# Kernel tuning notes

Measured on AMD Instinct MI355X. Metric: run time of the kernel, lower is better.

The kernel has to match this reference:

```python
import jax, jax.numpy as jnp
import numpy as np

N = 50000
E = 800000
D_IN = 256
D1, D2, D3 = 256, 256, 128


def setup_inputs() -> dict:
    key = jax.random.key(0)
    ks = jax.random.split(key, 9)
    qe = jax.random.normal(ks[0], (N, D_IN), dtype=jnp.float32)
    obj = jax.random.normal(ks[1], (N, D_IN), dtype=jnp.float32)
    edge_index = jax.random.randint(ks[2], (2, E), 0, N, dtype=jnp.int64)
    def glorot(k, fan_in, fan_out):
        s = jnp.sqrt(6.0 / (fan_in + fan_out)).astype(jnp.float32)
        return jax.random.uniform(k, (fan_in, fan_out), jnp.float32, -s, s)
    return {
        "question_embedding": qe,
        "object_features": obj,
        "edge_index": edge_index,
        "W1": glorot(ks[3], D_IN, D1), "b1": jnp.zeros((D1,), jnp.float32),
        "W2": glorot(ks[4], D1, D2),  "b2": jnp.zeros((D2,), jnp.float32),
        "W3": glorot(ks[5], D2, D3),  "b3": jnp.zeros((D3,), jnp.float32),
    }


def _gcn_norm(edge_index, num_nodes):
    # PyG GCNConv default: add self-loops, symmetric normalization D^-1/2 (A+I) D^-1/2
    loop = jnp.arange(num_nodes, dtype=edge_index.dtype)
    row = jnp.concatenate([edge_index[0], loop])  # destination
    col = jnp.concatenate([edge_index[1], loop])  # source
    ones = jnp.ones(row.shape[0], dtype=jnp.float32)
    deg = jax.ops.segment_sum(ones, row, num_segments=num_nodes)
    dinv = jnp.where(deg > 0, jax.lax.rsqrt(deg), 0.0)
    norm = dinv[row] * dinv[col]  # [E+N]
    return row, col, norm


def _gcn_layer(x, W, b, row, col, norm, num_nodes):
    h = x @ W                                   # [N, d_out] dense transform first (smaller msgs)
    msgs = norm[:, None] * h[col]               # gather + scale: [E+N, d_out]
    out = jax.ops.segment_sum(msgs, row, num_segments=num_nodes)  # scatter-add
    return out + b


def reference(question_embedding, object_features, edge_index, W1, b1, W2, b2, W3, b3):
    # Hadamard fusion of question embedding with per-object features (MuRel-style)
    x = question_embedding * object_features
    row, col, norm = _gcn_norm(edge_index, N)
    x = jax.nn.relu(_gcn_layer(x, W1, b1, row, col, norm, N))
    x = jax.nn.relu(_gcn_layer(x, W2, b2, row, col, norm, N))
    x = _gcn_layer(x, W3, b3, row, col, norm, N)
    return x
```

## Files before the change

### kernel.cpp

```cpp
#include <hip/hip_runtime.h>
#include <cstdint>
#include <cstddef>

#define NN 50000
#define NE 800000
#define NBLK ((NN + 255) / 256)

typedef _Float16 f16x8 __attribute__((ext_vector_type(8)));
typedef _Float16 f16x4 __attribute__((ext_vector_type(4)));
typedef float f32x4 __attribute__((ext_vector_type(4)));

__device__ __forceinline__ int edge_at(const void* e, int is32, long long i) {
    return is32 ? ((const int*)e)[i] : (int)((const long long*)e)[i];
}

__global__ __launch_bounds__(64) void zero_flag_k(int* flag) {
    if (threadIdx.x == 0) *flag = 0;
}

__global__ __launch_bounds__(256) void detect_k(const int* __restrict__ w, int* __restrict__ flag) {
    int i = blockIdx.x * 256 + threadIdx.x;
    if (i < 1024 && w[2 * i + 1] != 0) atomicOr(flag, 1);
}

__global__ __launch_bounds__(256) void init_k(int* __restrict__ deg, int* __restrict__ cursor, int n) {
    int i = blockIdx.x * 256 + threadIdx.x;
    if (i < n) { deg[i] = 1; cursor[i] = 0; }
}

__global__ __launch_bounds__(256) void count_k(const void* __restrict__ edges,
                                               const int* __restrict__ flag,
                                               int* __restrict__ deg, int e) {
    int i = blockIdx.x * 256 + threadIdx.x;
    if (i < e) {
        int is32 = *flag;
        atomicAdd(&deg[edge_at(edges, is32, i)], 1);
    }
}

__global__ __launch_bounds__(256) void bh_k(const int* __restrict__ deg,
                                            int* __restrict__ bh, int n) {
    __shared__ int lh[1024];
    int t = threadIdx.x;
    for (int b = t; b < 1024; b += 256) lh[b] = 0;
    __syncthreads();
    int i = blockIdx.x * 256 + t;
    if (i < n) atomicAdd(&lh[min(deg[i], 1023)], 1);
    __syncthreads();
    for (int b = t; b < 1024; b += 256) bh[(size_t)blockIdx.x * 1024 + b] = lh[b];
}

__global__ __launch_bounds__(256) void btot_k(const int* __restrict__ bh,
                                              int* __restrict__ tot, int nb) {
    __shared__ int red[256];
    int b = blockIdx.x, t = threadIdx.x;
    int s = 0;
    for (int blk = t; blk < nb; blk += 256) s += bh[(size_t)blk * 1024 + b];
    red[t] = s;
    __syncthreads();
    for (int off = 128; off; off >>= 1) {
        if (t < off) red[t] += red[t + off];
        __syncthreads();
    }
    if (t == 0) tot[b] = red[0];
}

__global__ __launch_bounds__(1024) void hscan_k(const int* __restrict__ hist,
                                                int* __restrict__ bcur) {
    __shared__ int s[1024];
    int t = threadIdx.x;
    s[t] = hist[t];
    __syncthreads();
    for (int off = 1; off < 1024; off <<= 1) {
        int val = (t >= off) ? s[t - off] : 0;
        __syncthreads();
        s[t] += val;
        __syncthreads();
    }
    bcur[t] = (t == 0) ? 0 : s[t - 1];
}

__global__ __launch_bounds__(256) void bbase_k(int* __restrict__ bh,
                                               const int* __restrict__ bstart, int nb) {
    __shared__ int s[256];
    int b = blockIdx.x, t = threadIdx.x;
    int v = (t < nb) ? bh[(size_t)t * 1024 + b] : 0;
    s[t] = v;
    __syncthreads();
    for (int off = 1; off < 256; off <<= 1) {
        int x = (t >= off) ? s[t - off] : 0;
        __syncthreads();
        s[t] += x;
        __syncthreads();
    }
    int excl = (t == 0) ? 0 : s[t - 1];
    if (t < nb) bh[(size_t)t * 1024 + b] = bstart[b] + excl;
}

__global__ __launch_bounds__(256) void pscatter_k(const int* __restrict__ deg,
                                                  const int* __restrict__ bh,
                                                  int* __restrict__ perm,
                                                  int* __restrict__ inv_perm, int n) {
    __shared__ int lh[1024];
    int t = threadIdx.x;
    for (int b = t; b < 1024; b += 256) lh[b] = 0;
    __syncthreads();
    int i = blockIdx.x * 256 + t;
    int b = 0, r = 0;
    if (i < n) {
        b = min(deg[i], 1023);
        r = atomicAdd(&lh[b], 1);
    }
    __syncthreads();
    if (i < n) {
        int pos = bh[(size_t)blockIdx.x * 1024 + b] + r;
        perm[pos] = i;
        inv_perm[i] = pos;
    }
}

__global__ __launch_bounds__(256) void degs_k(const int* __restrict__ deg,
                                              const int* __restrict__ perm,
                                              int* __restrict__ deg_s,
                                              float* __restrict__ dinv_s, int n) {
    int i = blockIdx.x * 256 + threadIdx.x;
    if (i < n) {
        int d = deg[perm[i]];
        deg_s[i] = d;
        dinv_s[i] = rsqrtf((float)d);
    }
}

__global__ __launch_bounds__(256) void ppart_k(const int* __restrict__ deg,
                                               int* __restrict__ part, int n) {
    __shared__ int red[256];
    int t = threadIdx.x;
    int i = blockIdx.x * 256 + t;
    red[t] = (i < n) ? deg[i] - 1 : 0;
    __syncthreads();
    for (int off = 128; off; off >>= 1) {
        if (t < off) red[t] += red[t + off];
        __syncthreads();
    }
    if (t == 0) part[blockIdx.x] = red[0];
}

__global__ __launch_bounds__(256) void pscan1_k(int* __restrict__ part, int nb) {
    __shared__ int s[256];
    int t = threadIdx.x;
    s[t] = (t < nb) ? part[t] : 0;
    __syncthreads();
    for (int off = 1; off < 256; off <<= 1) {
        int v = (t >= off) ? s[t - off] : 0;
        __syncthreads();
        s[t] += v;
        __syncthreads();
    }
    if (t < nb) part[t] = (t == 0) ? 0 : s[t - 1];
}

__global__ __launch_bounds__(256) void pwrite_k(const int* __restrict__ deg,
                                                const int* __restrict__ part,
                                                int* __restrict__ rp, int n) {
    __shared__ int s[256];
    int t = threadIdx.x;
    int i = blockIdx.x * 256 + t;
    int val = (i < n) ? deg[i] - 1 : 0;
    s[t] = val;
    __syncthreads();
    for (int off = 1; off < 256; off <<= 1) {
        int v = (t >= off) ? s[t - off] : 0;
        __syncthreads();
        s[t] += v;
        __syncthreads();
    }
    int incl = s[t];
    if (i < n) rp[i] = part[blockIdx.x] + incl - val;
    if (i == n - 1) rp[n] = part[blockIdx.x] + incl;
}

__global__ __launch_bounds__(256) void scatter_k(const void* __restrict__ edges,
                                                 const int* __restrict__ flag,
                                                 const int* __restrict__ inv_perm,
                                                 const int* __restrict__ rp,
                                                 int* __restrict__ cursor,
                                                 unsigned short* __restrict__ col_s, int e) {
    int i = blockIdx.x * 256 + threadIdx.x;
    if (i < e) {
        int is32 = *flag;
        int r = inv_perm[edge_at(edges, is32, i)];
        int c = inv_perm[edge_at(edges, is32, (long long)NE + i)];
        int pos = rp[r] + atomicAdd(&cursor[r], 1);
        col_s[pos] = (unsigned short)c;
    }
}

__global__ __launch_bounds__(256) void hadamard_k(const float4* __restrict__ a,
                                                  const float4* __restrict__ b,
                                                  const int* __restrict__ perm,
                                                  _Float16* __restrict__ Xh,
                                                  _Float16* __restrict__ Xl, int n4) {
    int i = blockIdx.x * 256 + threadIdx.x;
    if (i >= n4) return;
    int slot = i >> 6;
    int q = i & 63;
    int v = perm[slot];
    float4 x = a[(size_t)v * 64 + q], y = b[(size_t)v * 64 + q];
    float vv[4] = { x.x * y.x, x.y * y.y, x.z * y.z, x.w * y.w };
    f16x4 hh, ll;
    #pragma unroll
    for (int j = 0; j < 4; ++j) {
        _Float16 h = (_Float16)vv[j];
        hh[j] = h;
        ll[j] = (_Float16)(vv[j] - (float)h);
    }
    int cq = q * 4;
    size_t off = ((size_t)(cq >> 5) * NN + slot) * 32 + (cq & 31);
    *(f16x4*)&Xh[off] = hh;
    *(f16x4*)&Xl[off] = ll;
}

__global__ __launch_bounds__(256) void wconv_k(const float* __restrict__ W,
                                               _Float16* __restrict__ B3,
                                               int Nout, int nseg) {
    int n = blockIdx.x;
    int k = threadIdx.x;
    float v = W[(size_t)k * Nout + n];
    _Float16 h = (_Float16)v;
    _Float16 l = (_Float16)(v - (float)h);
    size_t base = (size_t)n * (nseg * 256);
    B3[base + k]       = h;
    B3[base + 256 + k] = l;
    if (nseg == 3) B3[base + 512 + k] = h;
}

__device__ __forceinline__ void gload_lds16(const void* g, void* l) {
    __builtin_amdgcn_global_load_lds(
        (const __attribute__((address_space(1))) void*)g,
        (__attribute__((address_space(3))) void*)l, 16, 0, 0);
}

template <int NBX, int SW, int NSEG>
__global__ __launch_bounds__(256) void gemm_f16_k(const _Float16* __restrict__ Ah,
                                                  const _Float16* __restrict__ Al,
                                                  const _Float16* __restrict__ B3,
                                                  const float* __restrict__ dinv_s,
                                                  _Float16* __restrict__ C,
                                                  int M, int Nout) {
    __shared__ alignas(16) _Float16 sA[128 * 32];
    __shared__ alignas(16) _Float16 sB[128 * 32];
    constexpr int LG = (SW == 32) ? 5 : 4;
    constexpr int NST = NSEG * 8;
    constexpr int BSTR = NSEG * 256;
    int mblk = (M + 127) >> 7;

    int pair, xb;
    if (NBX == 2) {
        int b = blockIdx.x;
        pair = (b >> 4) * 8 + (b & 7);
        xb   = (b >> 3) & 1;
        if (pair >= mblk) return;
    } else {
        pair = blockIdx.x;
        xb = 0;
    }

    int tid = threadIdx.x;
    int row0 = pair * 128, col0 = xb * 128;
    int wid = tid >> 6, lane = tid & 63;
    int wm = wid >> 1, wn = wid & 1;
    int fr = lane & 15;
    int kbc = lane >> 4;

    int sr = lane >> 2;
    int ke = (((lane & 3) ^ ((sr >> 1) & 3)) * 8);

    f32x4 acc[4][4] = {};

    for (int s = 0; s < NST; ++s) {
        int p = s & 7;
        const _Float16* Asrc = Ah;
        if constexpr (NSEG == 3) {
            if ((s >> 3) == 2) Asrc = Al;
        }

        __syncthreads();
        #pragma unroll
        for (int c = 0; c < 2; ++c) {
            int ch = wid * 2 + c;
            int r = ch * 16 + sr;
            int arow = row0 + r;
            if (arow < M)
                gload_lds16(&Asrc[((size_t)p * M + arow) * 32 + ke], &sA[ch * 512]);
            gload_lds16(&B3[(size_t)(col0 + r) * BSTR + s * 32 + ke], &sB[ch * 512]);
        }
        __syncthreads();

        f16x8 af[4];
        #pragma unroll
        for (int f = 0; f < 4; ++f) {
            int rr = wm * 64 + f * 16 + fr;
            af[f] = *(const f16x8*)&sA[rr * 32 + ((kbc ^ ((rr >> 1) & 3)) * 8)];
        }
        #pragma unroll
        for (int g = 0; g < 4; ++g) {
            int cc = wn * 64 + g * 16 + fr;
            f16x8 bf_ = *(const f16x8*)&sB[cc * 32 + ((kbc ^ ((cc >> 1) & 3)) * 8)];
            #pragma unroll
            for (int f = 0; f < 4; ++f)
                acc[f][g] = __builtin_amdgcn_mfma_f32_16x16x32_f16(af[f], bf_, acc[f][g], 0, 0, 0);
        }
    }

    int rsub = (lane >> 4) * 4;
    float dsc[4][4];
    #pragma unroll
    for (int f = 0; f < 4; ++f)
        #pragma unroll
        for (int r = 0; r < 4; ++r) {
            int row = row0 + wm * 64 + f * 16 + rsub + r;
            dsc[f][r] = (row < M) ? dinv_s[row] : 0.0f;
        }
    #pragma unroll
    for (int f = 0; f < 4; ++f) {
        #pragma unroll
        for (int g = 0; g < 4; ++g) {
            int col = col0 + wn * 64 + g * 16 + fr;
            #pragma unroll
            for (int r = 0; r < 4; ++r) {
                int row = row0 + wm * 64 + f * 16 + rsub + r;
                if (row < M)
                    C[((size_t)(col >> LG) * M + row) * SW + (col & (SW - 1))] =
                        (_Float16)(acc[f][g][r] * dsc[f][r]);
            }
        }
    }
}

template <int D, int MODE>
__global__ __launch_bounds__(256) void aggregate_slice_k(const _Float16* __restrict__ G,
                                                         const float* __restrict__ bias,
                                                         const float* __restrict__ dinv_s,
                                                         const int* __restrict__ rp,
                                                         const unsigned short* __restrict__ cs,
                                                         const int* __restrict__ perm,
                                                         _Float16* __restrict__ Yh,
                                                         float* __restrict__ Yf, int n) {
    constexpr int SLICE = (D == 256) ? 32 : 16;
    constexpr int LPN = SLICE / 8;
    constexpr int NPB = 256 / LPN;

    int bid = blockIdx.x;
    int s = bid & 7;
    int slot = (bid >> 3) * NPB + threadIdx.x / LPN;
    if (slot >= n) return;
    int sub = threadIdx.x % LPN;
    int co = sub * 8;
    int col = s * SLICE + co;

    const _Float16* Gs = G + (size_t)s * n * SLICE;

    float acc[8];
    {
        f16x8 t0 = *(const f16x8*)&Gs[(size_t)slot * SLICE + co];
        #pragma unroll
        for (int i = 0; i < 8; ++i) acc[i] = (float)t0[i];
    }

    int beg = rp[slot], end = rp[slot + 1];
    int j = beg;
    for (; j + 8 <= end; j += 8) {
        int cc[8];
        #pragma unroll
        for (int u = 0; u < 8; ++u) cc[u] = cs[j + u];
        f16x8 hv[8];
        #pragma unroll
        for (int u = 0; u < 8; ++u)
            hv[u] = *(const f16x8*)&Gs[(size_t)cc[u] * SLICE + co];
        #pragma unroll
        for (int u = 0; u < 8; ++u)
            #pragma unroll
            for (int i = 0; i < 8; ++i)
                acc[i] += (float)hv[u][i];
    }
    for (; j < end; ++j) {
        int c = cs[j];
        f16x8 a = *(const f16x8*)&Gs[(size_t)c * SLICE + co];
        #pragma unroll
        for (int i = 0; i < 8; ++i) acc[i] += (float)a[i];
    }

    float dv = dinv_s[slot];
    float4 b0 = *(const float4*)&bias[col];
    float4 b1 = *(const float4*)&bias[col + 4];
    float bb[8] = { b0.x, b0.y, b0.z, b0.w, b1.x, b1.y, b1.z, b1.w };

    if constexpr (MODE == 0) {
        f16x8 hh;
        #pragma unroll
        for (int i = 0; i < 8; ++i)
            hh[i] = (_Float16)fmaxf(dv * acc[i] + bb[i], 0.0f);
        size_t off = ((size_t)s * n + slot) * SLICE + co;
        *(f16x8*)&Yh[off] = hh;
    } else {
        int v = perm[slot];
        float o[8];
        #pragma unroll
        for (int i = 0; i < 8; ++i) o[i] = dv * acc[i] + bb[i];
        *(float4*)&Yf[(size_t)v * D + col]     = make_float4(o[0], o[1], o[2], o[3]);
        *(float4*)&Yf[(size_t)v * D + col + 4] = make_float4(o[4], o[5], o[6], o[7]);
    }
}

extern "C" void kernel_launch(void* const* d_in, const int* in_sizes, int n_in,
                              void* d_out, int out_size, void* d_ws, size_t ws_size,
                              hipStream_t stream) {
    const float* qe  = (const float*)d_in[0];
    const float* obj = (const float*)d_in[1];
    const void*  edges = d_in[2];
    const float* W1 = (const float*)d_in[3];
    const float* b1 = (const float*)d_in[4];
    const float* W2 = (const float*)d_in[5];
    const float* b2 = (const float*)d_in[6];
    const float* W3 = (const float*)d_in[7];
    const float* b3 = (const float*)d_in[8];
    float* out = (float*)d_out;

    char* p = (char*)d_ws;
    _Float16* Xh   = (_Float16*)p; p += (size_t)NN * 256 * 2;
    _Float16* Xl   = (_Float16*)p; p += (size_t)NN * 256 * 2;
    _Float16* H    = (_Float16*)p; p += (size_t)NN * 256 * 2;
    _Float16* B3   = (_Float16*)p; p += (size_t)256 * 768 * 2;
    int*   deg     = (int*)p;   p += (size_t)NN * 4;
    int*   deg_s   = (int*)p;   p += (size_t)NN * 4;
    float* dinv_s  = (float*)p; p += (size_t)NN * 4;
    int*   rp      = (int*)p;   p += (size_t)(NN + 1) * 4;
    int*   cursor  = (int*)p;   p += (size_t)NN * 4;
    unsigned short* col_s = (unsigned short*)p; p += (size_t)NE * 2;
    int*   bh      = (int*)p;   p += (size_t)NBLK * 1024 * 4;
    int*   tot     = (int*)p;   p += 1024 * 4;
    int*   bstart  = (int*)p;   p += 1024 * 4;
    int*   part    = (int*)p;   p += NBLK * 4;
    int*   perm    = (int*)p;   p += (size_t)NN * 4;
    int*   inv_perm= (int*)p;   p += (size_t)NN * 4;
    int*   flag    = (int*)p;   p += 4;

    zero_flag_k<<<1, 64, 0, stream>>>(flag);
    detect_k<<<4, 256, 0, stream>>>((const int*)edges, flag);
    init_k<<<(NN + 255) / 256, 256, 0, stream>>>(deg, cursor, NN);
    count_k<<<(NE + 255) / 256, 256, 0, stream>>>(edges, flag, deg, NE);
    bh_k<<<NBLK, 256, 0, stream>>>(deg, bh, NN);
    btot_k<<<1024, 256, 0, stream>>>(bh, tot, NBLK);
    hscan_k<<<1, 1024, 0, stream>>>(tot, bstart);
    bbase_k<<<1024, 256, 0, stream>>>(bh, bstart, NBLK);
    pscatter_k<<<NBLK, 256, 0, stream>>>(deg, bh, perm, inv_perm, NN);
    degs_k<<<NBLK, 256, 0, stream>>>(deg, perm, deg_s, dinv_s, NN);
    ppart_k<<<NBLK, 256, 0, stream>>>(deg_s, part, NN);
    pscan1_k<<<1, 256, 0, stream>>>(part, NBLK);
    pwrite_k<<<NBLK, 256, 0, stream>>>(deg_s, part, rp, NN);
    scatter_k<<<(NE + 255) / 256, 256, 0, stream>>>(edges, flag, inv_perm, rp, cursor,
                                                    col_s, NE);
    hadamard_k<<<(NN * 64 + 255) / 256, 256, 0, stream>>>(
        (const float4*)qe, (const float4*)obj, perm, Xh, Xl, NN * 64);

    int mblk = (NN + 127) / 128;
    int gemmBigGrid = ((mblk + 7) / 8) * 16;
    int agg256Grid = ((NN + 63) / 64) * 8;
    int agg128Grid = ((NN + 127) / 128) * 8;

    wconv_k<<<256, 256, 0, stream>>>(W1, B3, 256, 3);
    gemm_f16_k<2, 32, 3><<<gemmBigGrid, 256, 0, stream>>>(Xh, Xl, B3, dinv_s, H, NN, 256);
    aggregate_slice_k<256, 0><<<agg256Grid, 256, 0, stream>>>(H, b1, dinv_s, rp, col_s, perm,
                                                              Xh, nullptr, NN);
    wconv_k<<<256, 256, 0, stream>>>(W2, B3, 256, 2);
    gemm_f16_k<2, 32, 2><<<gemmBigGrid, 256, 0, stream>>>(Xh, nullptr, B3, dinv_s, H, NN, 256);
    aggregate_slice_k<256, 0><<<agg256Grid, 256, 0, stream>>>(H, b2, dinv_s, rp, col_s, perm,
                                                              Xh, nullptr, NN);
    wconv_k<<<128, 256, 0, stream>>>(W3, B3, 128, 2);
    gemm_f16_k<1, 16, 2><<<mblk, 256, 0, stream>>>(Xh, nullptr, B3, dinv_s, H, NN, 128);
    aggregate_slice_k<128, 1><<<agg128Grid, 256, 0, stream>>>(H, b3, dinv_s, rp, col_s, perm,
                                                              nullptr, out, NN);
}
```

Measured before the change: 356.5 us.

## Drop low-half activation split in layer 1 and double-buffer GEMM LDS stages

Result: faster. 342.7 us (-3.9%).

```diff
diff --git a/kernel.cpp b/kernel.cpp
--- a/kernel.cpp
+++ b/kernel.cpp
@@ -198,40 +198,31 @@
 __global__ __launch_bounds__(256) void hadamard_k(const float4* __restrict__ a,
                                                   const float4* __restrict__ b,
                                                   const int* __restrict__ perm,
-                                                  _Float16* __restrict__ Xh,
-                                                  _Float16* __restrict__ Xl, int n4) {
+                                                  _Float16* __restrict__ Xh, int n4) {
     int i = blockIdx.x * 256 + threadIdx.x;
     if (i >= n4) return;
     int slot = i >> 6;
     int q = i & 63;
     int v = perm[slot];
     float4 x = a[(size_t)v * 64 + q], y = b[(size_t)v * 64 + q];
-    float vv[4] = { x.x * y.x, x.y * y.y, x.z * y.z, x.w * y.w };
-    f16x4 hh, ll;
-    #pragma unroll
-    for (int j = 0; j < 4; ++j) {
-        _Float16 h = (_Float16)vv[j];
-        hh[j] = h;
-        ll[j] = (_Float16)(vv[j] - (float)h);
-    }
+    f16x4 hh;
+    hh[0] = (_Float16)(x.x * y.x);
+    hh[1] = (_Float16)(x.y * y.y);
+    hh[2] = (_Float16)(x.z * y.z);
+    hh[3] = (_Float16)(x.w * y.w);
     int cq = q * 4;
     size_t off = ((size_t)(cq >> 5) * NN + slot) * 32 + (cq & 31);
     *(f16x4*)&Xh[off] = hh;
-    *(f16x4*)&Xl[off] = ll;
 }
 
 __global__ __launch_bounds__(256) void wconv_k(const float* __restrict__ W,
-                                               _Float16* __restrict__ B3,
-                                               int Nout, int nseg) {
+                                               _Float16* __restrict__ B3, int Nout) {
     int n = blockIdx.x;
     int k = threadIdx.x;
     float v = W[(size_t)k * Nout + n];
     _Float16 h = (_Float16)v;
-    _Float16 l = (_Float16)(v - (float)h);
-    size_t base = (size_t)n * (nseg * 256);
-    B3[base + k]       = h;
-    B3[base + 256 + k] = l;
-    if (nseg == 3) B3[base + 512 + k] = h;
+    B3[(size_t)n * 512 + k]       = h;
+    B3[(size_t)n * 512 + 256 + k] = (_Float16)(v - (float)h);
 }
 
 __device__ __forceinline__ void gload_lds16(const void* g, void* l) {
@@ -240,18 +231,16 @@
         (__attribute__((address_space(3))) void*)l, 16, 0, 0);
 }
 
-template <int NBX, int SW, int NSEG>
+template <int NBX, int SW>
 __global__ __launch_bounds__(256) void gemm_f16_k(const _Float16* __restrict__ Ah,
-                                                  const _Float16* __restrict__ Al,
                                                   const _Float16* __restrict__ B3,
                                                   const float* __restrict__ dinv_s,
                                                   _Float16* __restrict__ C,
                                                   int M, int Nout) {
-    __shared__ alignas(16) _Float16 sA[128 * 32];
-    __shared__ alignas(16) _Float16 sB[128 * 32];
+    __shared__ alignas(16) _Float16 sA[2][128 * 32];
+    __shared__ alignas(16) _Float16 sB[2][128 * 32];
     constexpr int LG = (SW == 32) ? 5 : 4;
-    constexpr int NST = NSEG * 8;
-    constexpr int BSTR = NSEG * 256;
+    constexpr int NST = 16;
     int mblk = (M + 127) >> 7;
 
     int pair, xb;
@@ -277,39 +266,43 @@
 
     f32x4 acc[4][4] = {};
 
-    for (int s = 0; s < NST; ++s) {
+    auto STAGE = [&](int bsel, int s) {
         int p = s & 7;
-        const _Float16* Asrc = Ah;
-        if constexpr (NSEG == 3) {
-            if ((s >> 3) == 2) Asrc = Al;
-        }
-
-        __syncthreads();
         #pragma unroll
         for (int c = 0; c < 2; ++c) {
             int ch = wid * 2 + c;
             int r = ch * 16 + sr;
             int arow = row0 + r;
             if (arow < M)
-                gload_lds16(&Asrc[((size_t)p * M + arow) * 32 + ke], &sA[ch * 512]);
-            gload_lds16(&B3[(size_t)(col0 + r) * BSTR + s * 32 + ke], &sB[ch * 512]);
+                gload_lds16(&Ah[((size_t)p * M + arow) * 32 + ke], &sA[bsel][ch * 512]);
+            gload_lds16(&B3[(size_t)(col0 + r) * 512 + s * 32 + ke], &sB[bsel][ch * 512]);
         }
-        __syncthreads();
+    };
+
+    STAGE(0, 0);
+    __syncthreads();
+    int cur = 0;
+
+    for (int s = 0; s < NST; ++s) {
+        if (s + 1 < NST) STAGE(cur ^ 1, s + 1);
 
         f16x8 af[4];
         #pragma unroll
         for (int f = 0; f < 4; ++f) {
             int rr = wm * 64 + f * 16 + fr;
-            af[f] = *(const f16x8*)&sA[rr * 32 + ((kbc ^ ((rr >> 1) & 3)) * 8)];
+            af[f] = *(const f16x8*)&sA[cur][rr * 32 + ((kbc ^ ((rr >> 1) & 3)) * 8)];
         }
         #pragma unroll
         for (int g = 0; g < 4; ++g) {
             int cc = wn * 64 + g * 16 + fr;
-            f16x8 bf_ = *(const f16x8*)&sB[cc * 32 + ((kbc ^ ((cc >> 1) & 3)) * 8)];
+            f16x8 bf_ = *(const f16x8*)&sB[cur][cc * 32 + ((kbc ^ ((cc >> 1) & 3)) * 8)];
             #pragma unroll
             for (int f = 0; f < 4; ++f)
                 acc[f][g] = __builtin_amdgcn_mfma_f32_16x16x32_f16(af[f], bf_, acc[f][g], 0, 0, 0);
         }
+
+        __syncthreads();
+        cur ^= 1;
     }
 
     int rsub = (lane >> 4) * 4;
@@ -428,9 +421,8 @@
 
     char* p = (char*)d_ws;
     _Float16* Xh   = (_Float16*)p; p += (size_t)NN * 256 * 2;
-    _Float16* Xl   = (_Float16*)p; p += (size_t)NN * 256 * 2;
     _Float16* H    = (_Float16*)p; p += (size_t)NN * 256 * 2;
-    _Float16* B3   = (_Float16*)p; p += (size_t)256 * 768 * 2;
+    _Float16* B3   = (_Float16*)p; p += (size_t)256 * 512 * 2;
     int*   deg     = (int*)p;   p += (size_t)NN * 4;
     int*   deg_s   = (int*)p;   p += (size_t)NN * 4;
     float* dinv_s  = (float*)p; p += (size_t)NN * 4;
@@ -461,23 +453,23 @@
     scatter_k<<<(NE + 255) / 256, 256, 0, stream>>>(edges, flag, inv_perm, rp, cursor,
                                                     col_s, NE);
     hadamard_k<<<(NN * 64 + 255) / 256, 256, 0, stream>>>(
-        (const float4*)qe, (const float4*)obj, perm, Xh, Xl, NN * 64);
+        (const float4*)qe, (const float4*)obj, perm, Xh, NN * 64);
 
     int mblk = (NN + 127) / 128;
     int gemmBigGrid = ((mblk + 7) / 8) * 16;
     int agg256Grid = ((NN + 63) / 64) * 8;
     int agg128Grid = ((NN + 127) / 128) * 8;
 
-    wconv_k<<<256, 256, 0, stream>>>(W1, B3, 256, 3);
-    gemm_f16_k<2, 32, 3><<<gemmBigGrid, 256, 0, stream>>>(Xh, Xl, B3, dinv_s, H, NN, 256);
+    wconv_k<<<256, 256, 0, stream>>>(W1, B3, 256);
+    gemm_f16_k<2, 32><<<gemmBigGrid, 256, 0, stream>>>(Xh, B3, dinv_s, H, NN, 256);
     aggregate_slice_k<256, 0><<<agg256Grid, 256, 0, stream>>>(H, b1, dinv_s, rp, col_s, perm,
                                                               Xh, nullptr, NN);
-    wconv_k<<<256, 256, 0, stream>>>(W2, B3, 256, 2);
-    gemm_f16_k<2, 32, 2><<<gemmBigGrid, 256, 0, stream>>>(Xh, nullptr, B3, dinv_s, H, NN, 256);
+    wconv_k<<<256, 256, 0, stream>>>(W2, B3, 256);
+    gemm_f16_k<2, 32><<<gemmBigGrid, 256, 0, stream>>>(Xh, B3, dinv_s, H, NN, 256);
     aggregate_slice_k<256, 0><<<agg256Grid, 256, 0, stream>>>(H, b2, dinv_s, rp, col_s, perm,
                                                               Xh, nullptr, NN);
-    wconv_k<<<128, 256, 0, stream>>>(W3, B3, 128, 2);
-    gemm_f16_k<1, 16, 2><<<mblk, 256, 0, stream>>>(Xh, nullptr, B3, dinv_s, H, NN, 128);
+    wconv_k<<<128, 256, 0, stream>>>(W3, B3, 128);
+    gemm_f16_k<1, 16><<<mblk, 256, 0, stream>>>(Xh, B3, dinv_s, H, NN, 128);
     aggregate_slice_k<128, 1><<<agg128Grid, 256, 0, stream>>>(H, b3, dinv_s, rp, col_s, perm,
                                                               nullptr, out, NN);
 }
```
